# Kernel optimization log

Measured on AMD Instinct MI355X. Metric: run time of the kernel, lower is better.

Reference implementation:

```python
import jax, jax.numpy as jnp
import numpy as np

N = 100000   # num visited nodes
D = 128      # emb_dim
B = 1024     # num queries (eg_idx groups)
DEG = 256    # edges per query group (fixed, > K so topk always prunes)
E = B * DEG  # 262144 edges
K = 20       # max_attended_edges
RATIO = 0.0  # ratio_update
NEG_SLOPE = 0.01  # LeakyReLU default


def segment_softmax(logits, seg, num_segments):
    m = jax.ops.segment_max(logits, seg, num_segments=num_segments)
    ex = jnp.exp(logits - m[seg])
    s = jax.ops.segment_sum(ex, seg, num_segments=num_segments)
    return ex / s[seg]


def setup_inputs() -> dict:
    key = jax.random.key(0)
    ks = jax.random.split(key, 11)
    node_score = jax.random.uniform(ks[0], (N,), dtype=jnp.float32)
    node_repr = jax.random.normal(ks[1], (N, D), dtype=jnp.float32)
    rel_emb = jax.random.normal(ks[2], (E, D), dtype=jnp.float32)
    q_src_emb = jax.random.normal(ks[3], (B, D), dtype=jnp.float32)
    q_rel_emb = jax.random.normal(ks[4], (B, D), dtype=jnp.float32)
    # G3: Linear(4D, 4D, bias=False), init normal std sqrt(2/dim_in)
    Wq = jax.random.normal(ks[5], (4 * D, 4 * D), dtype=jnp.float32) * np.sqrt(2.0 / (4 * D))
    Wk = jax.random.normal(ks[6], (4 * D, 4 * D), dtype=jnp.float32) * np.sqrt(2.0 / (4 * D))
    # linear_between_steps: Linear(D, D) xavier
    W_lin = jax.random.normal(ks[7], (D, D), dtype=jnp.float32) * np.sqrt(2.0 / (2 * D))
    b_lin = jnp.zeros((D,), dtype=jnp.float32)
    # edges: [E, 8]; col0 = eg_idx (sorted, fixed DEG per group), col6 = vi, col7 = vj
    eg = jnp.repeat(jnp.arange(B, dtype=jnp.int32), DEG)
    vi = jax.random.randint(ks[8], (E,), 0, N, dtype=jnp.int32)
    vj = jax.random.randint(ks[9], (E,), 0, N, dtype=jnp.int32)
    z = jnp.zeros((E,), dtype=jnp.int32)
    edges = jnp.stack([eg, z, z, z, z, z, vi, vj], axis=1)
    return {
        "node_score": node_score, "node_repr": node_repr, "rel_emb": rel_emb,
        "q_src_emb": q_src_emb, "q_rel_emb": q_rel_emb,
        "Wq": Wq, "Wk": Wk, "W_lin": W_lin, "b_lin": b_lin, "edges": edges,
    }


def reference(node_score, node_repr, rel_emb, q_src_emb, q_rel_emb, Wq, Wk, W_lin, b_lin, edges):
    eg = edges[:, 0]
    vi = edges[:, 6]
    vj = edges[:, 7]
    # --- G3 attention score over edges ---
    hvi = node_repr[vi]           # [E, D]
    hvj = node_repr[vj]           # [E, D]
    qst = q_src_emb[eg]           # [E, D]
    qr = q_rel_emb[eg]            # [E, D]
    left = jnp.concatenate([hvi, rel_emb, qst, qr], axis=-1)   # [E, 4D]
    right = jnp.concatenate([hvj, rel_emb, qst, qr], axis=-1)  # [E, 4D]
    logits = jnp.sum((left @ Wq.T) * (right @ Wk.T), axis=-1)  # [E]
    # --- segment softmax over source node vi ---
    sm = segment_softmax(logits, vi, N)
    src_score = node_score[vi]
    target_score = sm * src_score
    # --- per-query-group top-k edge pruning (fixed DEG per group) ---
    topk_vals, topk_idx = jax.lax.top_k(target_score.reshape(B, DEG), K)  # [B, K]
    flat_idx = (topk_idx + jnp.arange(B, dtype=topk_idx.dtype)[:, None] * DEG).reshape(-1)  # [B*K]
    p_vi = vi[flat_idx]
    p_vj = vj[flat_idx]
    p_sm = sm[flat_idx]
    p_src = src_score[flat_idx]
    # --- node score aggregation: scatter-sum sm*src_score into target node vj ---
    updated_node_score = jax.ops.segment_sum(p_sm * p_src, p_vj, num_segments=N)
    # --- node representation update (sparse transition + identity fill) ---
    agg = jax.ops.segment_sum((1.0 - RATIO) * p_sm[:, None] * node_repr[p_vj], p_vi, num_segments=N)
    appears = jnp.zeros((N,), dtype=jnp.float32).at[p_vi].set(1.0)
    self_coef = jnp.where(appears > 0, RATIO, 1.0)[:, None]
    updated_repr = agg + self_coef * node_repr
    # --- bypass_forward: LeakyReLU(Linear) ---
    updated_repr = jax.nn.leaky_relu(updated_repr @ W_lin.T + b_lin, NEG_SLOPE)
    return updated_node_score, updated_repr
```

## Files before the change

kernel.cpp:

```cpp
#include <hip/hip_runtime.h>

#define NN 100000
#define BQ 1024
#define EE 262144
#define KTOP 20

typedef unsigned long long ull;
typedef __attribute__((ext_vector_type(8))) short bf16x8;
typedef __attribute__((ext_vector_type(4))) float f32x4;

__device__ __forceinline__ ull enc64(double d) {
  ull u = (ull)__double_as_longlong(d);
  return (u >> 63) ? ~u : (u | 0x8000000000000000ull);
}
__device__ __forceinline__ double dec64(ull u) {
  ull b = (u >> 63) ? (u & 0x7FFFFFFFFFFFFFFFull) : ~u;
  return __longlong_as_double((long long)b);
}

__device__ __forceinline__ unsigned short f2bf(float f) {
  unsigned u = __float_as_uint(f);
  u += 0x7fff + ((u >> 16) & 1);
  return (unsigned short)(u >> 16);
}
__device__ __forceinline__ float bf2f(unsigned short h) {
  return __uint_as_float(((unsigned)h) << 16);
}
__device__ __forceinline__ void cvt8(float4 x, float4 y, bf16x8& hi, bf16x8& lo) {
  float a[8] = {x.x, x.y, x.z, x.w, y.x, y.y, y.z, y.w};
#pragma unroll
  for (int j = 0; j < 8; j++) {
    unsigned short h = f2bf(a[j]);
    float r = a[j] - bf2f(h);
    hi[j] = (short)h;
    lo[j] = (short)f2bf(r);
  }
}

__global__ void k_prep(const int* __restrict__ edges, int4* __restrict__ evi,
                       int* __restrict__ vi32, ull* __restrict__ menc,
                       double* __restrict__ s, float* __restrict__ appears,
                       float* __restrict__ out_score) {
  int i = blockIdx.x * 256 + threadIdx.x;
  int st = gridDim.x * 256;
  for (int e = i; e < EE; e += st) {
    int vi = edges[(size_t)e * 8 + 6];
    evi[e] = make_int4(edges[(size_t)e * 8 + 0], vi, edges[(size_t)e * 8 + 7], 0);
    vi32[e] = vi;
  }
  for (int n = i; n < NN; n += st) {
    menc[n] = 0ull;
    s[n] = 0.0;
    appears[n] = 0.f;
    out_score[n] = 0.f;
  }
}

__global__ void k_matM(const float* __restrict__ Wq, const float* __restrict__ Wk,
                       float* __restrict__ M, float* __restrict__ MT) {
  int x = blockIdx.x;
  int y = blockIdx.y * 256 + threadIdx.x;
  float acc = 0.f;
  for (int a = 0; a < 512; a++)
    acc += Wq[a * 512 + x] * Wk[a * 512 + y];
  M[x * 512 + y] = acc;
  MT[y * 512 + x] = acc;
}

__global__ void k_pack(const float* __restrict__ M, const float* __restrict__ MT,
                       const float* __restrict__ Wl,
                       short* __restrict__ wn_hi, short* __restrict__ wn_lo,
                       short* __restrict__ m11_hi, short* __restrict__ m11_lo,
                       short* __restrict__ wl_hi, short* __restrict__ wl_lo) {
  int idx = blockIdx.x * 256 + threadIdx.x;
  if (idx >= 5 * 16384) return;
  int arr = idx >> 14;
  int j16 = idx & 16383;
  int g = j16 >> 9;
  int l = (j16 >> 3) & 63;
  int jj = j16 & 7;
  int c = (g >> 2) * 16 + (l & 15);
  int k = (g & 3) * 32 + ((l >> 4) << 3) + jj;
  float v;
  short *dh, *dl;
  if (arr == 0)      { v = MT[(size_t)c * 512 + k];               dh = wn_hi;          dl = wn_lo; }
  else if (arr == 1) { v = MT[(size_t)(128 + c) * 512 + k];       dh = wn_hi + 16384;  dl = wn_lo + 16384; }
  else if (arr == 2) { v = M[(size_t)(128 + c) * 512 + k];        dh = wn_hi + 32768;  dl = wn_lo + 32768; }
  else if (arr == 3) { v = MT[(size_t)(128 + c) * 512 + 128 + k]; dh = m11_hi;         dl = m11_lo; }
  else               { v = Wl[(size_t)c * 128 + k];               dh = wl_hi;          dl = wl_lo; }
  unsigned short h = f2bf(v);
  float r = v - bf2f(h);
  dh[j16] = (short)h;
  dl[j16] = (short)f2bf(r);
}

__global__ void k_pq(const float* __restrict__ M, const float* __restrict__ MT,
                     const float* __restrict__ qsA, const float* __restrict__ qrA,
                     float* __restrict__ Qv, double* __restrict__ cq) {
  int b = blockIdx.x, d = threadIdx.x;
  __shared__ float qs[128], qr[128];
  qs[d] = qsA[b * 128 + d];
  qr[d] = qrA[b * 128 + d];
  __syncthreads();
  float uh = 0, ui = 0, ur = 0;
  for (int x = 0; x < 128; x++) {
    float qsx = qs[x], qrx = qr[x];
    uh += qsx * M[(256 + x) * 512 + d]        + qrx * M[(384 + x) * 512 + d];
    ur += qsx * M[(256 + x) * 512 + 128 + d]  + qrx * M[(384 + x) * 512 + 128 + d];
    ui += qsx * MT[(256 + x) * 512 + d]       + qrx * MT[(384 + x) * 512 + d];
    ur += qsx * MT[(256 + x) * 512 + 128 + d] + qrx * MT[(384 + x) * 512 + 128 + d];
  }
  Qv[b * 384 + d]       = uh;
  Qv[b * 384 + 128 + d] = ui;
  Qv[b * 384 + 256 + d] = ur;
  float t1 = 0, t2 = 0;
  for (int y = 0; y < 128; y++) {
    float qsy = qs[y], qry = qr[y];
    t1 += qsy * MT[(256 + y) * 512 + 256 + d] + qry * MT[(384 + y) * 512 + 256 + d];
    t2 += qsy * MT[(256 + y) * 512 + 384 + d] + qry * MT[(384 + y) * 512 + 384 + d];
  }
  float cp = qs[d] * t1 + qr[d] * t2;
  for (int off = 32; off; off >>= 1) cp += __shfl_down(cp, off, 64);
  __shared__ float red[2];
  if ((d & 63) == 0) red[d >> 6] = cp;
  __syncthreads();
  if (d == 0) cq[b] = (double)(red[0] + red[1]);
}

__global__ __launch_bounds__(512) void k_gemm_node(const float* __restrict__ A,
                                                   const short* __restrict__ WT_hi,
                                                   const short* __restrict__ WT_lo,
                                                   float* __restrict__ G,
                                                   float* __restrict__ H1,
                                                   float* __restrict__ J) {
  __shared__ __align__(16) float As[64][132];
  __shared__ __align__(16) short Bh[16384];
  float* Of = (float*)Bh;
  int t = threadIdx.x;
  int row0 = blockIdx.x * 64;
  int w = t >> 6, l = t & 63;
  int rt = w & 3;
  int c0 = (w >> 2) * 4;
#pragma unroll
  for (int i = 0; i < 4; i++) {
    int fi = t + i * 512;
    int r = fi >> 5, c4 = (fi & 31) * 4;
    float4 v = make_float4(0.f, 0.f, 0.f, 0.f);
    if (row0 + r < NN) v = *(const float4*)(A + (size_t)(row0 + r) * 128 + c4);
    *(float4*)&As[r][c4] = v;
    *(bf16x8*)&Bh[fi * 8] = *(const bf16x8*)(WT_hi + fi * 8);
  }
  __syncthreads();
  int rloc = rt * 16 + (l & 15);
  int kq = (l >> 4) * 8;
  for (int panel = 0; panel < 3; panel++) {
    const short* sl = WT_lo + panel * 16384;
    bf16x8 blv[4][4];
#pragma unroll
    for (int cc = 0; cc < 4; cc++)
#pragma unroll
      for (int kt = 0; kt < 4; kt++)
        blv[cc][kt] = *(const bf16x8*)(sl + (((c0 + cc) * 4 + kt) * 64 + l) * 8);
    f32x4 acc[4];
#pragma unroll
    for (int cc = 0; cc < 4; cc++)
#pragma unroll
      for (int j = 0; j < 4; j++) acc[cc][j] = 0.f;
#pragma unroll
    for (int kt = 0; kt < 4; kt++) {
      int kb = kt * 32 + kq;
      float4 x = *(const float4*)&As[rloc][kb];
      float4 y = *(const float4*)&As[rloc][kb + 4];
      bf16x8 ah, al;
      cvt8(x, y, ah, al);
#pragma unroll
      for (int cc = 0; cc < 4; cc++) {
        int off = (((cc + c0) * 4 + kt) * 64 + l) * 8;
        bf16x8 bhv = *(const bf16x8*)&Bh[off];
        acc[cc] = __builtin_amdgcn_mfma_f32_16x16x32_bf16(ah, bhv, acc[cc], 0, 0, 0);
        acc[cc] = __builtin_amdgcn_mfma_f32_16x16x32_bf16(al, bhv, acc[cc], 0, 0, 0);
        acc[cc] = __builtin_amdgcn_mfma_f32_16x16x32_bf16(ah, blv[cc][kt], acc[cc], 0, 0, 0);
      }
    }
    __syncthreads();
#pragma unroll
    for (int cc = 0; cc < 4; cc++) {
      int col = (c0 + cc) * 16 + (l & 15);
#pragma unroll
      for (int reg = 0; reg < 4; reg++)
        Of[(rt * 16 + (l >> 4) * 4 + reg) * 128 + col] = acc[cc][reg];
    }
    __syncthreads();
    float* dst = (panel == 0) ? G : (panel == 1) ? H1 : J;
#pragma unroll
    for (int i = 0; i < 4; i++) {
      int fi = t + i * 512;
      int r = fi >> 5, c4 = (fi & 31) * 4;
      int rr = row0 + r;
      if (rr < NN) *(float4*)&dst[(size_t)rr * 128 + c4] = *(float4*)&Of[r * 128 + c4];
    }
    if (panel < 2) {
      __syncthreads();
      const short* sh = WT_hi + (panel + 1) * 16384;
#pragma unroll
      for (int i = 0; i < 4; i++) {
        int fi = t + i * 512;
        *(bf16x8*)&Bh[fi * 8] = *(const bf16x8*)(sh + fi * 8);
      }
      __syncthreads();
    }
  }
}

__global__ __launch_bounds__(512, 1) void k_edge(const float* __restrict__ rel,
                                                 const short* __restrict__ M11T_hi,
                                                 const short* __restrict__ M11T_lo,
                                                 const int4* __restrict__ evi,
                                                 const float* __restrict__ H1,
                                                 const float* __restrict__ J,
                                                 const float* __restrict__ Qv,
                                                 float* __restrict__ rq) {
  __shared__ __align__(16) float Rs[64][132];
  __shared__ __align__(16) short Bh[16384];
  __shared__ float part[2][64];
  __shared__ float dg[64];
  __shared__ float urs[128];
  int t = threadIdx.x;
  int e0 = blockIdx.x * 64;
  int eg = e0 >> 8;
  int w = t >> 6, l = t & 63;
  int rt = w & 3;
  int h = w >> 2;
  bf16x8 blv[4][4];
#pragma unroll
  for (int cc = 0; cc < 4; cc++)
#pragma unroll
    for (int kt = 0; kt < 4; kt++)
      blv[cc][kt] = *(const bf16x8*)(M11T_lo + (((h * 4 + cc) * 4 + kt) * 64 + l) * 8);
#pragma unroll
  for (int i = 0; i < 4; i++) {
    int fi = t + i * 512;
    int r = fi >> 5, c4 = (fi & 31) * 4;
    *(float4*)&Rs[r][c4] = *(const float4*)(rel + (size_t)(e0 + r) * 128 + c4);
    *(bf16x8*)&Bh[fi * 8] = *(const bf16x8*)(M11T_hi + fi * 8);
  }
  if (t < 128) urs[t] = Qv[(size_t)eg * 384 + 256 + t];
  __syncthreads();
  int kq = (l >> 4) * 8;
  int rloc = rt * 16 + (l & 15);
  f32x4 acc[4];
#pragma unroll
  for (int cc = 0; cc < 4; cc++)
#pragma unroll
    for (int j = 0; j < 4; j++) acc[cc][j] = 0.f;
#pragma unroll
  for (int kt = 0; kt < 4; kt++) {
    int kb = kt * 32 + kq;
    float4 x = *(const float4*)&Rs[rloc][kb];
    float4 y = *(const float4*)&Rs[rloc][kb + 4];
    bf16x8 ah, al;
    cvt8(x, y, ah, al);
#pragma unroll
    for (int cc = 0; cc < 4; cc++) {
      bf16x8 bhv = *(const bf16x8*)&Bh[(((h * 4 + cc) * 4 + kt) * 64 + l) * 8];
      acc[cc] = __builtin_amdgcn_mfma_f32_16x16x32_bf16(ah, bhv, acc[cc], 0, 0, 0);
      acc[cc] = __builtin_amdgcn_mfma_f32_16x16x32_bf16(al, bhv, acc[cc], 0, 0, 0);
      acc[cc] = __builtin_amdgcn_mfma_f32_16x16x32_bf16(ah, blv[cc][kt], acc[cc], 0, 0, 0);
    }
  }
  int rq4 = (l >> 4) * 4;
  float p[4] = {0.f, 0.f, 0.f, 0.f};
#pragma unroll
  for (int cc = 0; cc < 4; cc++) {
    int c = (h * 4 + cc) * 16 + (l & 15);
#pragma unroll
    for (int reg = 0; reg < 4; reg++)
      p[reg] += acc[cc][reg] * Rs[rt * 16 + rq4 + reg][c];
  }
#pragma unroll
  for (int reg = 0; reg < 4; reg++) {
    p[reg] += __shfl_xor(p[reg], 1, 64);
    p[reg] += __shfl_xor(p[reg], 2, 64);
    p[reg] += __shfl_xor(p[reg], 4, 64);
    p[reg] += __shfl_xor(p[reg], 8, 64);
  }
  if ((l & 15) == 0) {
#pragma unroll
    for (int reg = 0; reg < 4; reg++) part[h][rt * 16 + rq4 + reg] = p[reg];
  }
  int gg = t >> 4;
  int ll = t & 15;
  int d = ll * 8;
  float4 u0 = *(const float4*)&urs[d], u1 = *(const float4*)&urs[d + 4];
#pragma unroll
  for (int pe = 0; pe < 2; pe++) {
    int le = gg * 2 + pe;
    int e = e0 + le;
    int4 ed = evi[e];
    const float* h1p = H1 + (size_t)ed.y * 128 + d;
    const float* jp  = J + (size_t)ed.z * 128 + d;
    float4 a0 = *(const float4*)h1p, a1 = *(const float4*)(h1p + 4);
    float4 b0 = *(const float4*)jp,  b1 = *(const float4*)(jp + 4);
    float4 r0 = *(const float4*)&Rs[le][d], r1 = *(const float4*)&Rs[le][d + 4];
    float dot = (a0.x + b0.x + u0.x) * r0.x + (a0.y + b0.y + u0.y) * r0.y
              + (a0.z + b0.z + u0.z) * r0.z + (a0.w + b0.w + u0.w) * r0.w
              + (a1.x + b1.x + u1.x) * r1.x + (a1.y + b1.y + u1.y) * r1.y
              + (a1.z + b1.z + u1.z) * r1.z + (a1.w + b1.w + u1.w) * r1.w;
    dot += __shfl_xor(dot, 1, 64);
    dot += __shfl_xor(dot, 2, 64);
    dot += __shfl_xor(dot, 4, 64);
    dot += __shfl_xor(dot, 8, 64);
    if (ll == 0) dg[le] = dot;
  }
  __syncthreads();
  if (t < 64) rq[e0 + t] = (part[0][t] + part[1][t]) + dg[t];
}

__global__ __launch_bounds__(256) void k_logits(const int4* __restrict__ evi,
                                                const float* __restrict__ nrep,
                                                const float* __restrict__ G,
                                                const float* __restrict__ Qv,
                                                const double* __restrict__ cq,
                                                const float* __restrict__ rq,
                                                double* __restrict__ logits,
                                                ull* __restrict__ menc) {
  int t = threadIdx.x;
  int ll = t & 15;
  int grp = (t & 63) >> 4;
  int wid = blockIdx.x * 4 + (t >> 6);
  int nw = gridDim.x * 4;
  int d = ll * 8;
  for (int e4 = wid; e4 < EE / 4; e4 += nw) {
    int e = e4 * 4 + grp;
    int4 ed = evi[e];
    int eg = ed.x, vi = ed.y, vj = ed.z;
    const float* gp = G + (size_t)vi * 128 + d;
    const float* hi = nrep + (size_t)vi * 128 + d;
    const float* hj = nrep + (size_t)vj * 128 + d;
    const float* q  = Qv + (size_t)eg * 384 + d;
    float4 g0  = *(const float4*)gp,        g1  = *(const float4*)(gp + 4);
    float4 a0  = *(const float4*)hi,        a1  = *(const float4*)(hi + 4);
    float4 b0  = *(const float4*)hj,        b1  = *(const float4*)(hj + 4);
    float4 uh0 = *(const float4*)q,         uh1 = *(const float4*)(q + 4);
    float4 ui0 = *(const float4*)(q + 128), ui1 = *(const float4*)(q + 132);
    float acc;
    acc  = (g0.x + uh0.x) * b0.x + (g0.y + uh0.y) * b0.y
         + (g0.z + uh0.z) * b0.z + (g0.w + uh0.w) * b0.w
         + (g1.x + uh1.x) * b1.x + (g1.y + uh1.y) * b1.y
         + (g1.z + uh1.z) * b1.z + (g1.w + uh1.w) * b1.w;
    acc += ui0.x * a0.x + ui0.y * a0.y + ui0.z * a0.z + ui0.w * a0.w
         + ui1.x * a1.x + ui1.y * a1.y + ui1.z * a1.z + ui1.w * a1.w;
    acc += __shfl_xor(acc, 1, 64);
    acc += __shfl_xor(acc, 2, 64);
    acc += __shfl_xor(acc, 4, 64);
    acc += __shfl_xor(acc, 8, 64);
    if (ll == 0) {
      double l2 = (double)acc + cq[eg] + (double)rq[e];
      logits[e] = l2;
      atomicMax(&menc[vi], enc64(l2));
    }
  }
}

__global__ void k_exp(const int* __restrict__ vi32, const ull* __restrict__ menc,
                      const double* __restrict__ logits, double* __restrict__ ex,
                      double* __restrict__ s, float4* __restrict__ agg) {
  int i = blockIdx.x * 256 + threadIdx.x;
  int st = gridDim.x * 256;
  for (int e = i; e < EE; e += st) {
    int vi = vi32[e];
    double m = dec64(menc[vi]);
    double v = exp(logits[e] - m);
    ex[e] = v;
    atomicAdd(&s[vi], v);
  }
  const int n4 = NN * 32;
  for (int n = i; n < n4; n += st) agg[n] = make_float4(0.f, 0.f, 0.f, 0.f);
}

__global__ void k_topk(const double* __restrict__ ex, const double* __restrict__ s,
                       const float* __restrict__ nscore, const int4* __restrict__ evi,
                       const float* __restrict__ nrep, float* __restrict__ out_score,
                       float* __restrict__ agg, float* __restrict__ appears) {
  int b = blockIdx.x, t = threadIdx.x;
  int e = b * 256 + t;
  int vi_t = evi[e].y;
  double v = ex[e] / s[vi_t] * (double)nscore[vi_t];
  __shared__ double cv[80];
  __shared__ int ci[80];
  __shared__ int winners[KTOP];
  int w = t >> 6;
  for (int k = 0; k < KTOP; k++) {
    double bv = v;
    int bi = t;
    for (int off = 32; off; off >>= 1) {
      double ov = __shfl_down(bv, off, 64);
      int oi = __shfl_down(bi, off, 64);
      if (ov > bv || (ov == bv && oi < bi)) { bv = ov; bi = oi; }
    }
    bi = __shfl(bi, 0, 64);
    if ((t & 63) == 0) { cv[w * KTOP + k] = bv; ci[w * KTOP + k] = bi; }
    if (t == bi) v = -1.0;
  }
  __syncthreads();
  if (t < 64) {
    double v0 = cv[t];
    int i0 = ci[t];
    double v1 = (t < 16) ? cv[64 + t] : -2.0;
    int i1 = (t < 16) ? ci[64 + t] : (1 << 30);
    for (int k = 0; k < KTOP; k++) {
      double bv; int bi;
      if (v1 > v0 || (v1 == v0 && i1 < i0)) { bv = v1; bi = i1; }
      else                                  { bv = v0; bi = i0; }
      for (int off = 32; off; off >>= 1) {
        double ov = __shfl_down(bv, off, 64);
        int oi = __shfl_down(bi, off, 64);
        if (ov > bv || (ov == bv && oi < bi)) { bv = ov; bi = oi; }
      }
      bi = __shfl(bi, 0, 64);
      if (t == 0) winners[k] = bi;
      if (i0 == bi) v0 = -2.0;
      if (i1 == bi) v1 = -2.0;
    }
  }
  __syncthreads();
  for (int k = 0; k < KTOP; k++) {
    int we = b * 256 + winners[k];
    int4 ew = evi[we];
    int vi = ew.y, vj = ew.z;
    double sm = ex[we] / s[vi];
    if (t < 128) {
      atomicAdd(&agg[(size_t)vi * 128 + t], (float)sm * nrep[(size_t)vj * 128 + t]);
    } else if (t == 128) {
      atomicAdd(&out_score[vj], (float)(sm * (double)nscore[vi]));
    } else if (t == 129) {
      appears[vi] = 1.f;
    }
  }
}

__global__ __launch_bounds__(512) void k_final(const float* __restrict__ agg,
                                               const float* __restrict__ appears,
                                               const float* __restrict__ nrep,
                                               const short* __restrict__ Wl_hi,
                                               const short* __restrict__ Wl_lo,
                                               const float* __restrict__ bl,
                                               float* __restrict__ outr) {
  __shared__ __align__(16) float Xs[64][132];
  __shared__ __align__(16) short Bh[16384];
  int t = threadIdx.x;
  int row0 = blockIdx.x * 64;
  int w = t >> 6, l = t & 63;
  int rt = w & 3;
  int c0 = (w >> 2) * 4;
  bf16x8 blv[4][4];
#pragma unroll
  for (int cc = 0; cc < 4; cc++)
#pragma unroll
    for (int kt = 0; kt < 4; kt++)
      blv[cc][kt] = *(const bf16x8*)(Wl_lo + (((c0 + cc) * 4 + kt) * 64 + l) * 8);
#pragma unroll
  for (int i = 0; i < 4; i++) {
    int fi = t + i * 512;
    int r = fi >> 5, c4 = (fi & 31) * 4;
    int rr = row0 + r;
    float4 v = make_float4(0.f, 0.f, 0.f, 0.f);
    if (rr < NN) {
      float4 ag = *(const float4*)(agg + (size_t)rr * 128 + c4);
      float4 h = *(const float4*)(nrep + (size_t)rr * 128 + c4);
      float coef = (appears[rr] > 0.f) ? 0.f : 1.f;
      v.x = ag.x + coef * h.x;
      v.y = ag.y + coef * h.y;
      v.z = ag.z + coef * h.z;
      v.w = ag.w + coef * h.w;
    }
    *(float4*)&Xs[r][c4] = v;
    *(bf16x8*)&Bh[fi * 8] = *(const bf16x8*)(Wl_hi + fi * 8);
  }
  __syncthreads();
  int rloc = rt * 16 + (l & 15);
  int kq = (l >> 4) * 8;
  f32x4 acc[4];
#pragma unroll
  for (int cc = 0; cc < 4; cc++)
#pragma unroll
    for (int j = 0; j < 4; j++) acc[cc][j] = 0.f;
#pragma unroll
  for (int kt = 0; kt < 4; kt++) {
    int kb = kt * 32 + kq;
    float4 x = *(const float4*)&Xs[rloc][kb];
    float4 y = *(const float4*)&Xs[rloc][kb + 4];
    bf16x8 ah, al;
    cvt8(x, y, ah, al);
#pragma unroll
    for (int cc = 0; cc < 4; cc++) {
      int off = (((c0 + cc) * 4 + kt) * 64 + l) * 8;
      bf16x8 bhv = *(const bf16x8*)&Bh[off];
      acc[cc] = __builtin_amdgcn_mfma_f32_16x16x32_bf16(ah, bhv, acc[cc], 0, 0, 0);
      acc[cc] = __builtin_amdgcn_mfma_f32_16x16x32_bf16(al, bhv, acc[cc], 0, 0, 0);
      acc[cc] = __builtin_amdgcn_mfma_f32_16x16x32_bf16(ah, blv[cc][kt], acc[cc], 0, 0, 0);
    }
  }
  __syncthreads();
#pragma unroll
  for (int cc = 0; cc < 4; cc++) {
    int col = (c0 + cc) * 16 + (l & 15);
#pragma unroll
    for (int reg = 0; reg < 4; reg++)
      Xs[rt * 16 + (l >> 4) * 4 + reg][col] = acc[cc][reg];
  }
  __syncthreads();
#pragma unroll
  for (int i = 0; i < 4; i++) {
    int fi = t + i * 512;
    int r = fi >> 5, c4 = (fi & 31) * 4;
    int rr = row0 + r;
    if (rr < NN) {
      float4 v = *(float4*)&Xs[r][c4];
      float4 bb = *(const float4*)&bl[c4];
      float4 o;
      o.x = v.x + bb.x; o.x = (o.x > 0.f) ? o.x : 0.01f * o.x;
      o.y = v.y + bb.y; o.y = (o.y > 0.f) ? o.y : 0.01f * o.y;
      o.z = v.z + bb.z; o.z = (o.z > 0.f) ? o.z : 0.01f * o.z;
      o.w = v.w + bb.w; o.w = (o.w > 0.f) ? o.w : 0.01f * o.w;
      *(float4*)&outr[(size_t)rr * 128 + c4] = o;
    }
  }
}

extern "C" void kernel_launch(void* const* d_in, const int* in_sizes, int n_in,
                              void* d_out, int out_size, void* d_ws, size_t ws_size,
                              hipStream_t stream) {
  const float* node_score = (const float*)d_in[0];
  const float* node_repr  = (const float*)d_in[1];
  const float* rel_emb    = (const float*)d_in[2];
  const float* q_src      = (const float*)d_in[3];
  const float* q_rel      = (const float*)d_in[4];
  const float* Wq         = (const float*)d_in[5];
  const float* Wk         = (const float*)d_in[6];
  const float* W_lin      = (const float*)d_in[7];
  const float* b_lin      = (const float*)d_in[8];
  const int*   edges      = (const int*)d_in[9];

  char* ws = (char*)d_ws;
  size_t off = 0;
  auto carve = [&](size_t bytes) -> void* {
    void* p = ws + off;
    off += (bytes + 255) & ~(size_t)255;
    return p;
  };
  float*  M      = (float*)carve(512 * 512 * 4);
  float*  MT     = (float*)carve(512 * 512 * 4);
  short*  wn_hi  = (short*)carve(3 * 16384 * 2);
  short*  wn_lo  = (short*)carve(3 * 16384 * 2);
  short*  m11_hi = (short*)carve(16384 * 2);
  short*  m11_lo = (short*)carve(16384 * 2);
  short*  wl_hi  = (short*)carve(16384 * 2);
  short*  wl_lo  = (short*)carve(16384 * 2);
  float*  Qv     = (float*)carve((size_t)BQ * 384 * 4);
  double* cq     = (double*)carve((size_t)BQ * 8);
  double* logits = (double*)carve((size_t)EE * 8);
  float*  rq     = (float*)carve((size_t)EE * 4);
  ull*    menc   = (ull*)carve((size_t)NN * 8);
  double* s      = (double*)carve((size_t)NN * 8);
  double* ex     = (double*)carve((size_t)EE * 8);
  float*  appears= (float*)carve((size_t)NN * 4);
  int4*   evi    = (int4*)carve((size_t)EE * 16);
  int*    vi32   = (int*)carve((size_t)EE * 4);
  float*  G      = (float*)carve((size_t)NN * 128 * 4);
  float*  H1     = (float*)carve((size_t)NN * 128 * 4);
  float*  J      = (float*)carve((size_t)NN * 128 * 4);
  float*  agg    = G;

  float* out_score = (float*)d_out;
  float* out_repr  = (float*)d_out + NN;

  k_prep<<<1024, 256, 0, stream>>>(edges, evi, vi32, menc, s, appears, out_score);
  k_matM<<<dim3(512, 2), 256, 0, stream>>>(Wq, Wk, M, MT);
  k_pack<<<320, 256, 0, stream>>>(M, MT, W_lin, wn_hi, wn_lo, m11_hi, m11_lo, wl_hi, wl_lo);
  k_pq<<<BQ, 128, 0, stream>>>(M, MT, q_src, q_rel, Qv, cq);
  k_gemm_node<<<1563, 512, 0, stream>>>(node_repr, wn_hi, wn_lo, G, H1, J);
  k_edge<<<4096, 512, 0, stream>>>(rel_emb, m11_hi, m11_lo, evi, H1, J, Qv, rq);
  k_logits<<<8192, 256, 0, stream>>>(evi, node_repr, G, Qv, cq, rq, logits, menc);
  k_exp<<<2048, 256, 0, stream>>>(vi32, menc, logits, ex, s, (float4*)agg);
  k_topk<<<BQ, 256, 0, stream>>>(ex, s, node_score, evi, node_repr, out_score, agg, appears);
  k_final<<<1563, 512, 0, stream>>>(agg, appears, node_repr, wl_hi, wl_lo, b_lin, out_repr);
}
```

Before: 388.0 us.

## Prefetch gathered H1/J rows before MFMA and remap waves to column quarters

In k_edge, the edge index reads and the gathered H1/J row loads are issued at kernel start, so their latency overlaps the shared-memory staging and MFMA work. The wave-to-tile mapping changes from 4 row tiles by 2 column halves to 2 row tiles by 4 column quarters. Each wave now loops over two row tiles, keeps half as many M11T_lo fragments in registers, and writes into a four-way partial-sum buffer. Keeping the prefetched rows live through the MFMA phase raises register pressure, and there is one more partial to add in the final sum.

```diff
diff --git a/kernel.cpp b/kernel.cpp
--- a/kernel.cpp
+++ b/kernel.cpp
@@ -222,21 +222,32 @@
                                                  float* __restrict__ rq) {
   __shared__ __align__(16) float Rs[64][132];
   __shared__ __align__(16) short Bh[16384];
-  __shared__ float part[2][64];
+  __shared__ float part[4][64];
   __shared__ float dg[64];
   __shared__ float urs[128];
   int t = threadIdx.x;
   int e0 = blockIdx.x * 64;
   int eg = e0 >> 8;
   int w = t >> 6, l = t & 63;
-  int rt = w & 3;
-  int h = w >> 2;
-  bf16x8 blv[4][4];
-#pragma unroll
-  for (int cc = 0; cc < 4; cc++)
+  int cq2 = w & 3;
+  int rh = w >> 2;
+  int gg = t >> 4, ll = t & 15, d = ll * 8;
+  int4 edA = evi[e0 + gg * 2];
+  int4 edB = evi[e0 + gg * 2 + 1];
+  const float* pA1 = H1 + (size_t)edA.y * 128 + d;
+  const float* pA2 = J + (size_t)edA.z * 128 + d;
+  const float* pB1 = H1 + (size_t)edB.y * 128 + d;
+  const float* pB2 = J + (size_t)edB.z * 128 + d;
+  float4 Aa0 = *(const float4*)pA1, Aa1 = *(const float4*)(pA1 + 4);
+  float4 Ab0 = *(const float4*)pA2, Ab1 = *(const float4*)(pA2 + 4);
+  float4 Ba0 = *(const float4*)pB1, Ba1 = *(const float4*)(pB1 + 4);
+  float4 Bb0 = *(const float4*)pB2, Bb1 = *(const float4*)(pB2 + 4);
+  bf16x8 blv[2][4];
+#pragma unroll
+  for (int cc = 0; cc < 2; cc++)
 #pragma unroll
     for (int kt = 0; kt < 4; kt++)
-      blv[cc][kt] = *(const bf16x8*)(M11T_lo + (((h * 4 + cc) * 4 + kt) * 64 + l) * 8);
+      blv[cc][kt] = *(const bf16x8*)(M11T_lo + (((cq2 * 2 + cc) * 4 + kt) * 64 + l) * 8);
 #pragma unroll
   for (int i = 0; i < 4; i++) {
     int fi = t + i * 512;
@@ -247,73 +258,81 @@
   if (t < 128) urs[t] = Qv[(size_t)eg * 384 + 256 + t];
   __syncthreads();
   int kq = (l >> 4) * 8;
-  int rloc = rt * 16 + (l & 15);
-  f32x4 acc[4];
-#pragma unroll
-  for (int cc = 0; cc < 4; cc++)
-#pragma unroll
-    for (int j = 0; j < 4; j++) acc[cc][j] = 0.f;
-#pragma unroll
-  for (int kt = 0; kt < 4; kt++) {
-    int kb = kt * 32 + kq;
-    float4 x = *(const float4*)&Rs[rloc][kb];
-    float4 y = *(const float4*)&Rs[rloc][kb + 4];
-    bf16x8 ah, al;
-    cvt8(x, y, ah, al);
-#pragma unroll
-    for (int cc = 0; cc < 4; cc++) {
-      bf16x8 bhv = *(const bf16x8*)&Bh[(((h * 4 + cc) * 4 + kt) * 64 + l) * 8];
-      acc[cc] = __builtin_amdgcn_mfma_f32_16x16x32_bf16(ah, bhv, acc[cc], 0, 0, 0);
-      acc[cc] = __builtin_amdgcn_mfma_f32_16x16x32_bf16(al, bhv, acc[cc], 0, 0, 0);
-      acc[cc] = __builtin_amdgcn_mfma_f32_16x16x32_bf16(ah, blv[cc][kt], acc[cc], 0, 0, 0);
-    }
-  }
   int rq4 = (l >> 4) * 4;
-  float p[4] = {0.f, 0.f, 0.f, 0.f};
-#pragma unroll
-  for (int cc = 0; cc < 4; cc++) {
-    int c = (h * 4 + cc) * 16 + (l & 15);
-#pragma unroll
-    for (int reg = 0; reg < 4; reg++)
-      p[reg] += acc[cc][reg] * Rs[rt * 16 + rq4 + reg][c];
-  }
-#pragma unroll
-  for (int reg = 0; reg < 4; reg++) {
-    p[reg] += __shfl_xor(p[reg], 1, 64);
-    p[reg] += __shfl_xor(p[reg], 2, 64);
-    p[reg] += __shfl_xor(p[reg], 4, 64);
-    p[reg] += __shfl_xor(p[reg], 8, 64);
-  }
-  if ((l & 15) == 0) {
-#pragma unroll
-    for (int reg = 0; reg < 4; reg++) part[h][rt * 16 + rq4 + reg] = p[reg];
-  }
-  int gg = t >> 4;
-  int ll = t & 15;
-  int d = ll * 8;
+#pragma unroll
+  for (int rt2 = 0; rt2 < 2; rt2++) {
+    int rt = rh * 2 + rt2;
+    int rloc = rt * 16 + (l & 15);
+    f32x4 acc[2];
+#pragma unroll
+    for (int cc = 0; cc < 2; cc++)
+#pragma unroll
+      for (int j = 0; j < 4; j++) acc[cc][j] = 0.f;
+#pragma unroll
+    for (int kt = 0; kt < 4; kt++) {
+      int kb = kt * 32 + kq;
+      float4 x = *(const float4*)&Rs[rloc][kb];
+      float4 y = *(const float4*)&Rs[rloc][kb + 4];
+      bf16x8 ah, al;
+      cvt8(x, y, ah, al);
+#pragma unroll
+      for (int cc = 0; cc < 2; cc++) {
+        bf16x8 bhv = *(const bf16x8*)&Bh[(((cq2 * 2 + cc) * 4 + kt) * 64 + l) * 8];
+        acc[cc] = __builtin_amdgcn_mfma_f32_16x16x32_bf16(ah, bhv, acc[cc], 0, 0, 0);
+        acc[cc] = __builtin_amdgcn_mfma_f32_16x16x32_bf16(al, bhv, acc[cc], 0, 0, 0);
+        acc[cc] = __builtin_amdgcn_mfma_f32_16x16x32_bf16(ah, blv[cc][kt], acc[cc], 0, 0, 0);
+      }
+    }
+    float p[4] = {0.f, 0.f, 0.f, 0.f};
+#pragma unroll
+    for (int cc = 0; cc < 2; cc++) {
+      int c = (cq2 * 2 + cc) * 16 + (l & 15);
+#pragma unroll
+      for (int reg = 0; reg < 4; reg++)
+        p[reg] += acc[cc][reg] * Rs[rt * 16 + rq4 + reg][c];
+    }
+#pragma unroll
+    for (int reg = 0; reg < 4; reg++) {
+      p[reg] += __shfl_xor(p[reg], 1, 64);
+      p[reg] += __shfl_xor(p[reg], 2, 64);
+      p[reg] += __shfl_xor(p[reg], 4, 64);
+      p[reg] += __shfl_xor(p[reg], 8, 64);
+    }
+    if ((l & 15) == 0) {
+#pragma unroll
+      for (int reg = 0; reg < 4; reg++) part[cq2][rt * 16 + rq4 + reg] = p[reg];
+    }
+  }
   float4 u0 = *(const float4*)&urs[d], u1 = *(const float4*)&urs[d + 4];
-#pragma unroll
-  for (int pe = 0; pe < 2; pe++) {
-    int le = gg * 2 + pe;
-    int e = e0 + le;
-    int4 ed = evi[e];
-    const float* h1p = H1 + (size_t)ed.y * 128 + d;
-    const float* jp  = J + (size_t)ed.z * 128 + d;
-    float4 a0 = *(const float4*)h1p, a1 = *(const float4*)(h1p + 4);
-    float4 b0 = *(const float4*)jp,  b1 = *(const float4*)(jp + 4);
+  {
+    int le = gg * 2;
     float4 r0 = *(const float4*)&Rs[le][d], r1 = *(const float4*)&Rs[le][d + 4];
-    float dot = (a0.x + b0.x + u0.x) * r0.x + (a0.y + b0.y + u0.y) * r0.y
-              + (a0.z + b0.z + u0.z) * r0.z + (a0.w + b0.w + u0.w) * r0.w
-              + (a1.x + b1.x + u1.x) * r1.x + (a1.y + b1.y + u1.y) * r1.y
-              + (a1.z + b1.z + u1.z) * r1.z + (a1.w + b1.w + u1.w) * r1.w;
+    float dot = (Aa0.x + Ab0.x + u0.x) * r0.x + (Aa0.y + Ab0.y + u0.y) * r0.y
+              + (Aa0.z + Ab0.z + u0.z) * r0.z + (Aa0.w + Ab0.w + u0.w) * r0.w
+              + (Aa1.x + Ab1.x + u1.x) * r1.x + (Aa1.y + Ab1.y + u1.y) * r1.y
+              + (Aa1.z + Ab1.z + u1.z) * r1.z + (Aa1.w + Ab1.w + u1.w) * r1.w;
     dot += __shfl_xor(dot, 1, 64);
     dot += __shfl_xor(dot, 2, 64);
     dot += __shfl_xor(dot, 4, 64);
     dot += __shfl_xor(dot, 8, 64);
     if (ll == 0) dg[le] = dot;
   }
-  __syncthreads();
-  if (t < 64) rq[e0 + t] = (part[0][t] + part[1][t]) + dg[t];
+  {
+    int le = gg * 2 + 1;
+    float4 r0 = *(const float4*)&Rs[le][d], r1 = *(const float4*)&Rs[le][d + 4];
+    float dot = (Ba0.x + Bb0.x + u0.x) * r0.x + (Ba0.y + Bb0.y + u0.y) * r0.y
+              + (Ba0.z + Bb0.z + u0.z) * r0.z + (Ba0.w + Bb0.w + u0.w) * r0.w
+              + (Ba1.x + Bb1.x + u1.x) * r1.x + (Ba1.y + Bb1.y + u1.y) * r1.y
+              + (Ba1.z + Bb1.z + u1.z) * r1.z + (Ba1.w + Bb1.w + u1.w) * r1.w;
+    dot += __shfl_xor(dot, 1, 64);
+    dot += __shfl_xor(dot, 2, 64);
+    dot += __shfl_xor(dot, 4, 64);
+    dot += __shfl_xor(dot, 8, 64);
+    if (ll == 0) dg[le] = dot;
+  }
+  __syncthreads();
+  if (t < 64)
+    rq[e0 + t] = ((part[0][t] + part[1][t]) + (part[2][t] + part[3][t])) + dg[t];
 }
 
 __global__ __launch_bounds__(256) void k_logits(const int4* __restrict__ evi,
```

Measured after the change: 380.6 us. About the same (-1.9%).
